# Kernel tuning notes

Hardware: AMD Instinct MI355X
Metric: run time of the kernel (lower is better)

The kernel has to match this reference:

```python
import jax, jax.numpy as jnp
import numpy as np

N_NODES = 100000
N_EDGES = 1600000
D_IN = 128
D_OUT = 128


def setup_inputs() -> dict:
    key = jax.random.key(0)
    k1, k2, k3, k4, k5 = jax.random.split(key, 5)
    x = jax.random.normal(k1, (N_NODES, D_IN), dtype=jnp.float32)
    edge_index = jax.random.randint(k2, (2, N_EDGES), 0, N_NODES, dtype=jnp.int32)
    edge_weight = jax.random.uniform(k3, (N_EDGES,), dtype=jnp.float32)
    # xavier-uniform linear weight [out, in]
    limit = float(np.sqrt(6.0 / (D_IN + D_OUT)))
    W = jax.random.uniform(k4, (D_OUT, D_IN), dtype=jnp.float32, minval=-limit, maxval=limit)
    bias = jnp.zeros((D_OUT,), dtype=jnp.float32)
    prelu_a = jax.random.uniform(k5, (1,), dtype=jnp.float32)
    return {"x": x, "edge_index": edge_index, "edge_weight": edge_weight,
            "W": W, "bias": bias, "prelu_a": prelu_a}


def _prelu(x, a):
    return jnp.where(x >= 0, x, a * x)


def reference(x, edge_index, edge_weight, W, bias, prelu_a):
    # seq_fts = fc(x): [N, D_OUT]
    h = x @ W.T
    # sparse adjacency matmul: out[dst] += w_e * h[src]
    src, dst = edge_index[0], edge_index[1]
    msgs = h[src] * edge_weight[:, None]          # [E, D_OUT]
    agg = jax.ops.segment_sum(msgs, dst, num_segments=N_NODES)
    out = agg + bias                              # bias add
    out = _prelu(out, prelu_a)                    # GCN's PReLU
    return jax.nn.relu(out)                       # GCNGeneration.activation
```

## Files before the change

kernel.cpp:

```cpp
#include <hip/hip_runtime.h>

#define N_NODES 100000
#define N_EDGES 1600000
#define D 128

#define NCB   512
#define BR    196
#define CHUNK 2048
#define SLOTS 8
#define CAP   4352

#define XQ   (N_NODES * D / 4)
#define XQB  (XQ / 256)
#define WQ   (D * D / 4)
#define WQB  (WQ / 256)
#define HB   256

typedef __bf16 bf16x8 __attribute__((ext_vector_type(8)));
typedef float  f32x4  __attribute__((ext_vector_type(4)));
typedef unsigned short u16x8 __attribute__((ext_vector_type(8)));

static __device__ __forceinline__ unsigned short f2bf(float f) {
    union { float f; unsigned u; } v; v.f = f;
    unsigned r = v.u + 0x7FFFu + ((v.u >> 16) & 1u);
    return (unsigned short)(r >> 16);
}

static __device__ __forceinline__ void accum_row(
    float4& acc0, float4& acc1, const float4 u, const float wt)
{
    const unsigned qx = __float_as_uint(u.x);
    const unsigned qy = __float_as_uint(u.y);
    const unsigned qz = __float_as_uint(u.z);
    const unsigned qw = __float_as_uint(u.w);
    acc0.x += wt * __uint_as_float(qx << 16);
    acc0.y += wt * __uint_as_float(qx & 0xFFFF0000u);
    acc0.z += wt * __uint_as_float(qy << 16);
    acc0.w += wt * __uint_as_float(qy & 0xFFFF0000u);
    acc1.x += wt * __uint_as_float(qz << 16);
    acc1.y += wt * __uint_as_float(qz & 0xFFFF0000u);
    acc1.z += wt * __uint_as_float(qw << 16);
    acc1.w += wt * __uint_as_float(qw & 0xFFFF0000u);
}

__global__ __launch_bounds__(256) void k_prep(
    const float4* __restrict__ x4, ushort4* __restrict__ xh4,
    const float4* __restrict__ w4, ushort4* __restrict__ wh4,
    const int* __restrict__ ei, int* __restrict__ ghist)
{
    __shared__ int h[NCB];
    const int b = blockIdx.x;
    const int t = threadIdx.x;
    if (b < HB) {
        h[t] = 0; h[t + 256] = 0;
        __syncthreads();
        for (int e = b * 256 + t; e < N_EDGES; e += HB * 256)
            atomicAdd(&h[ei[N_EDGES + e] / BR], 1);
        __syncthreads();
        atomicAdd(&ghist[t], h[t]);
        atomicAdd(&ghist[t + 256], h[t + 256]);
    } else if (b < HB + XQB) {
        const int i = (b - HB) * 256 + t;
        const float4 v = x4[i];
        xh4[i] = make_ushort4(f2bf(v.x), f2bf(v.y), f2bf(v.z), f2bf(v.w));
    } else {
        const int i = (b - HB - XQB) * 256 + t;
        const float4 v = w4[i];
        wh4[i] = make_ushort4(f2bf(v.x), f2bf(v.y), f2bf(v.z), f2bf(v.w));
    }
}

__global__ __launch_bounds__(512) void k_cscan(
    const int* __restrict__ ghist, int* __restrict__ cOff, int* __restrict__ gcur)
{
    __shared__ int sh[NCB];
    const int t = threadIdx.x;
    const int v = ghist[t];
    sh[t] = v;
    __syncthreads();
    for (int d = 1; d < NCB; d <<= 1) {
        int u = (t >= d) ? sh[t - d] : 0;
        __syncthreads();
        sh[t] += u;
        __syncthreads();
    }
    const int excl = sh[t] - v;
    cOff[t] = excl;
    gcur[t] = excl;
    if (t == NCB - 1) cOff[NCB] = sh[NCB - 1];
}

__global__ __launch_bounds__(256) void k_part(
    const int* __restrict__ ei, const float* __restrict__ ew,
    int* __restrict__ gcur, int2* __restrict__ part)
{
    __shared__ int2 bins[NCB * SLOTS];
    __shared__ int bcnt[NCB];
    __shared__ int bbase[NCB];
    const int t = threadIdx.x;
    const int e0 = blockIdx.x * CHUNK;

    bcnt[t] = 0; bcnt[t + 256] = 0;
    __syncthreads();

    #pragma unroll 8
    for (int k = 0; k < CHUNK / 256; ++k) {
        const int e = e0 + k * 256 + t;
        if (e < N_EDGES) {
            const int dst = ei[N_EDGES + e];
            const int src = ei[e];
            const int b = dst / BR;
            const int ld = dst - b * BR;
            const int2 p = make_int2(src | (ld << 17), __float_as_int(ew[e]));
            const int r = atomicAdd(&bcnt[b], 1);
            if (r < SLOTS) bins[b * SLOTS + r] = p;
            else {
                int pos = atomicAdd(&gcur[b], 1);
                part[pos] = p;
            }
        }
    }
    __syncthreads();

    {
        int c0 = min(bcnt[t], SLOTS);
        int c1 = min(bcnt[t + 256], SLOTS);
        bbase[t]       = c0 ? atomicAdd(&gcur[t], c0) : 0;
        bbase[t + 256] = c1 ? atomicAdd(&gcur[t + 256], c1) : 0;
        bcnt[t] = c0; bcnt[t + 256] = c1;
    }
    __syncthreads();

    for (int s = t; s < NCB * SLOTS; s += 256) {
        const int b = s >> 3;
        const int r = s & 7;
        if (r < bcnt[b]) part[bbase[b] + r] = bins[s];
    }
}

__global__ __launch_bounds__(256) void k_csr(
    const int* __restrict__ cOff, int2* __restrict__ part, int* __restrict__ off)
{
    __shared__ int2 buf[CAP];
    __shared__ int nh[256];
    __shared__ int orig[256];
    __shared__ int cur[256];

    const int b = blockIdx.x;
    const int t = threadIdx.x;
    const int lo = b * BR;
    const int base = cOff[b];
    int cnt = cOff[b + 1] - base;
    if (cnt > CAP) cnt = CAP;

    nh[t] = 0;
    __syncthreads();

    for (int i = t; i < cnt; i += 256) {
        const int2 p = part[base + i];
        buf[i] = p;
        atomicAdd(&nh[((unsigned)p.x) >> 17], 1);
    }
    __syncthreads();
    orig[t] = nh[t];
    __syncthreads();
    for (int d = 1; d < 256; d <<= 1) {
        int u = (t >= d) ? nh[t - d] : 0;
        __syncthreads();
        nh[t] += u;
        __syncthreads();
    }
    const int excl = nh[t] - orig[t];
    cur[t] = excl;
    if (t < BR && lo + t < N_NODES) off[lo + t] = base + excl;
    if (b == NCB - 1 && t == 0) off[N_NODES] = cOff[NCB];
    __syncthreads();

    for (int i = t; i < cnt; i += 256) {
        const int2 p = buf[i];
        const int ld = ((unsigned)p.x) >> 17;
        const int r = atomicAdd(&cur[ld], 1);
        part[base + r] = make_int2(p.x & 0x1FFFF, p.y);
    }
}

__global__ __launch_bounds__(256) void k_gx(
    const float4* __restrict__ xh4,
    const int* __restrict__ off,
    const int2* __restrict__ pair,
    const unsigned short* __restrict__ wh,
    const float* __restrict__ bias, const float* __restrict__ pa,
    float* __restrict__ out)
{
    __shared__ unsigned short tb[16][136];

    const int tid = threadIdx.x;
    const int g   = tid >> 4;
    const int sl  = tid & 15;
    const int m0  = blockIdx.x << 4;
    const float aP = pa[0];

    {
        const int n = m0 + g;
        const int beg = off[n], end = off[n + 1];
        float4 acc0 = make_float4(0.f, 0.f, 0.f, 0.f);
        float4 acc1 = make_float4(0.f, 0.f, 0.f, 0.f);

        int e = beg;
        for (; e + 3 < end; e += 4) {
            const int2 p0 = pair[e + 0], p1 = pair[e + 1];
            const int2 p2 = pair[e + 2], p3 = pair[e + 3];
            const float4 u0 = xh4[p0.x * 16 + sl];
            const float4 u1 = xh4[p1.x * 16 + sl];
            const float4 u2 = xh4[p2.x * 16 + sl];
            const float4 u3 = xh4[p3.x * 16 + sl];
            accum_row(acc0, acc1, u0, __int_as_float(p0.y));
            accum_row(acc0, acc1, u1, __int_as_float(p1.y));
            accum_row(acc0, acc1, u2, __int_as_float(p2.y));
            accum_row(acc0, acc1, u3, __int_as_float(p3.y));
        }
        for (; e < end; ++e) {
            const int2 p = pair[e];
            const float4 u = xh4[p.x * 16 + sl];
            accum_row(acc0, acc1, u, __int_as_float(p.y));
        }

        u16x8 s;
        s[0] = f2bf(acc0.x); s[1] = f2bf(acc0.y);
        s[2] = f2bf(acc0.z); s[3] = f2bf(acc0.w);
        s[4] = f2bf(acc1.x); s[5] = f2bf(acc1.y);
        s[6] = f2bf(acc1.z); s[7] = f2bf(acc1.w);
        *(u16x8*)&tb[g][sl * 8] = s;
    }
    __syncthreads();

    const int lane = tid & 63;
    const int wv = tid >> 6;
    const int mm = lane & 15;
    const int quad = lane >> 4;

    bf16x8 af[4];
    #pragma unroll
    for (int c = 0; c < 4; ++c)
        af[c] = *(const bf16x8*)&tb[mm][c * 32 + quad * 8];

    #pragma unroll
    for (int t = 0; t < 2; ++t) {
        const int n = ((wv * 2 + t) << 4) + mm;
        f32x4 acc = {0.f, 0.f, 0.f, 0.f};
        #pragma unroll
        for (int c = 0; c < 4; ++c) {
            const bf16x8 bf = *(const bf16x8*)(wh + n * D + c * 32 + quad * 8);
            acc = __builtin_amdgcn_mfma_f32_16x16x32_bf16(af[c], bf, acc, 0, 0, 0);
        }
        const float bv = bias[n];
        #pragma unroll
        for (int r = 0; r < 4; ++r) {
            float v = acc[r] + bv;
            v = (v >= 0.f) ? v : aP * v;
            v = fmaxf(v, 0.f);
            out[(size_t)(m0 + (quad << 2) + r) * D + n] = v;
        }
    }
}

__global__ __launch_bounds__(256) void gcn_scatter(
    const float* __restrict__ x, const int* __restrict__ ei,
    const float* __restrict__ ew, float* __restrict__ agg)
{
    const int lane = threadIdx.x & 63;
    const int wave = (blockIdx.x * blockDim.x + threadIdx.x) >> 6;
    const int nwaves = (gridDim.x * blockDim.x) >> 6;
    for (int e = wave; e < N_EDGES; e += nwaves) {
        const int src = ei[e];
        const int dst = ei[N_EDGES + e];
        const float w = ew[e];
        const float2 v = ((const float2*)(x + (size_t)src * D))[lane];
        float* op = agg + (size_t)dst * D + lane * 2;
        unsafeAtomicAdd(op,     w * v.x);
        unsafeAtomicAdd(op + 1, w * v.y);
    }
}

#define MT 32
__global__ __launch_bounds__(256, 2) void gcn_transform(
    const float* __restrict__ A, const float* __restrict__ W,
    const float* __restrict__ bias, const float* __restrict__ pa,
    float* __restrict__ out)
{
    __shared__ float Wt[D][D];
    __shared__ float xs[MT][D];
    const int tid = threadIdx.x;
    const int row0 = blockIdx.x * MT;

    for (int j = tid; j < D * (D / 4); j += 256) {
        const int n = j & 127;
        const int kg = j >> 7;
        const float4 v = ((const float4*)W)[n * (D / 4) + kg];
        const int k4 = kg << 2;
        Wt[k4 + 0][n] = v.x; Wt[k4 + 1][n] = v.y;
        Wt[k4 + 2][n] = v.z; Wt[k4 + 3][n] = v.w;
    }
    for (int i = tid; i < MT * (D / 4); i += 256) {
        const int r = i >> 5;
        const int c4 = i & 31;
        ((float4*)xs[r])[c4] = ((const float4*)(A + (size_t)(row0 + r) * D))[c4];
    }
    __syncthreads();

    const int tn = tid & 31;
    const int tm = tid >> 5;
    float acc[4][4] = {};
    #pragma unroll
    for (int k = 0; k < D; k += 4) {
        const float4 wv0 = *(const float4*)&Wt[k + 0][tn * 4];
        const float4 wv1 = *(const float4*)&Wt[k + 1][tn * 4];
        const float4 wv2 = *(const float4*)&Wt[k + 2][tn * 4];
        const float4 wv3 = *(const float4*)&Wt[k + 3][tn * 4];
        #pragma unroll
        for (int i = 0; i < 4; ++i) {
            const float4 xv = *(const float4*)&xs[tm * 4 + i][k];
            acc[i][0] += xv.x * wv0.x + xv.y * wv1.x + xv.z * wv2.x + xv.w * wv3.x;
            acc[i][1] += xv.x * wv0.y + xv.y * wv1.y + xv.z * wv2.y + xv.w * wv3.y;
            acc[i][2] += xv.x * wv0.z + xv.y * wv1.z + xv.z * wv2.z + xv.w * wv3.z;
            acc[i][3] += xv.x * wv0.w + xv.y * wv1.w + xv.z * wv2.w + xv.w * wv3.w;
        }
    }
    const float a = pa[0];
    const float4 bv = ((const float4*)bias)[tn];
    #pragma unroll
    for (int i = 0; i < 4; ++i) {
        const int gr = row0 + tm * 4 + i;
        float t0 = acc[i][0] + bv.x, t1 = acc[i][1] + bv.y;
        float t2 = acc[i][2] + bv.z, t3 = acc[i][3] + bv.w;
        float4 r;
        r.x = fmaxf(t0 >= 0.f ? t0 : a * t0, 0.f);
        r.y = fmaxf(t1 >= 0.f ? t1 : a * t1, 0.f);
        r.z = fmaxf(t2 >= 0.f ? t2 : a * t2, 0.f);
        r.w = fmaxf(t3 >= 0.f ? t3 : a * t3, 0.f);
        ((float4*)(out + (size_t)gr * D))[tn] = r;
    }
}

extern "C" void kernel_launch(void* const* d_in, const int* in_sizes, int n_in,
                              void* d_out, int out_size, void* d_ws, size_t ws_size,
                              hipStream_t stream) {
    const float* x    = (const float*)d_in[0];
    const int*   ei   = (const int*)d_in[1];
    const float* ew   = (const float*)d_in[2];
    const float* W    = (const float*)d_in[3];
    const float* bias = (const float*)d_in[4];
    const float* pa   = (const float*)d_in[5];
    float* out = (float*)d_out;

    const size_t o_ghist = 0;
    const size_t o_cOff  = o_ghist + NCB;
    const size_t o_gcur  = o_cOff + NCB + 1;
    const size_t o_off   = o_gcur + NCB;
    const size_t o_part  = o_off + N_NODES + 1;
    const size_t o_wh    = (o_part + 2 * (size_t)N_EDGES + 3) & ~(size_t)3;
    const size_t o_xh    = o_wh + (size_t)D * D / 2;
    const size_t endA    = o_xh + (size_t)N_NODES * D / 2;
    const size_t needA   = endA * 4;

    int* wsb = (int*)d_ws;
    int* ghist = wsb + o_ghist;
    int* cOff  = wsb + o_cOff;
    int* gcur  = wsb + o_gcur;
    int* off   = wsb + o_off;
    int2* part = (int2*)(wsb + o_part);
    unsigned short* wh = (unsigned short*)(wsb + o_wh);
    unsigned short* xh = (unsigned short*)(wsb + o_xh);

    if (ws_size >= needA) {
        (void)hipMemsetAsync(ghist, 0, NCB * sizeof(int), stream);
        k_prep <<<HB + XQB + WQB, 256, 0, stream>>>(
            (const float4*)x, (ushort4*)xh, (const float4*)W, (ushort4*)wh, ei, ghist);
        k_cscan<<<1, NCB, 0, stream>>>(ghist, cOff, gcur);
        k_part <<<(N_EDGES + CHUNK - 1) / CHUNK, 256, 0, stream>>>(ei, ew, gcur, part);
        k_csr  <<<NCB, 256, 0, stream>>>(cOff, part, off);
        k_gx   <<<N_NODES / 16, 256, 0, stream>>>(
            (const float4*)xh, off, part, wh, bias, pa, out);
    } else {
        (void)hipMemsetAsync(out, 0, (size_t)N_NODES * D * sizeof(float), stream);
        gcn_scatter<<<12800, 256, 0, stream>>>(x, ei, ew, out);
        gcn_transform<<<N_NODES / MT, 256, 0, stream>>>(out, W, bias, pa, out);
    }
}
```

Measured before the change: 267.5 us.

## Partition edges into fixed-capacity buckets to drop histogram and scan passes

Edges are binned by destination block straight into fixed-capacity per-bucket regions (CAPR slots each), so the separate destination histogram pass and the single-block prefix scan are no longer needed. Partitioning now runs in the same launch as the bf16 conversion of x and W. The CSR offsets become (begin,end) int2 pairs. This removes two kernel launches and one full read of the destination indices, but needs a larger workspace and silently drops edges if any bucket exceeds its capacity.

```diff
diff --git a/kernel.cpp b/kernel.cpp
--- a/kernel.cpp
+++ b/kernel.cpp
@@ -8,7 +8,10 @@
 #define BR    196
 #define CHUNK 2048
 #define SLOTS 8
+#define CAPR  4096
 #define CAP   4352
+#define LASTB ((N_NODES - 1) / BR)
+#define PBK   ((N_EDGES + CHUNK - 1) / CHUNK)
 
 #define XQ   (N_NODES * D / 4)
 #define XQB  (XQ / 256)
@@ -43,6 +46,114 @@
     acc1.w += wt * __uint_as_float(qw & 0xFFFF0000u);
 }
 
+
+__global__ __launch_bounds__(256) void k_pc(
+    const float4* __restrict__ x4, ushort4* __restrict__ xh4,
+    const float4* __restrict__ w4, ushort4* __restrict__ wh4,
+    const int* __restrict__ ei, const float* __restrict__ ew,
+    int* __restrict__ gcur, int2* __restrict__ part)
+{
+    __shared__ int2 bins[NCB * SLOTS];
+    __shared__ int bcnt[NCB];
+    __shared__ int bbase[NCB];
+    const int b = blockIdx.x;
+    const int t = threadIdx.x;
+
+    if (b < PBK) {
+        bcnt[t] = 0; bcnt[t + 256] = 0;
+        __syncthreads();
+        const int e0 = b * CHUNK;
+        #pragma unroll 8
+        for (int k = 0; k < CHUNK / 256; ++k) {
+            const int e = e0 + k * 256 + t;
+            if (e < N_EDGES) {
+                const int dst = ei[N_EDGES + e];
+                const int src = ei[e];
+                const int bk = dst / BR;
+                const int ld = dst - bk * BR;
+                const int2 p = make_int2(src | (ld << 17), __float_as_int(ew[e]));
+                const int r = atomicAdd(&bcnt[bk], 1);
+                if (r < SLOTS) bins[bk * SLOTS + r] = p;
+                else {
+                    const int pos = atomicAdd(&gcur[bk], 1);
+                    if (pos < CAPR) part[bk * CAPR + pos] = p;
+                }
+            }
+        }
+        __syncthreads();
+        {
+            const int c0 = min(bcnt[t], SLOTS);
+            const int c1 = min(bcnt[t + 256], SLOTS);
+            bbase[t]       = c0 ? atomicAdd(&gcur[t], c0) : 0;
+            bbase[t + 256] = c1 ? atomicAdd(&gcur[t + 256], c1) : 0;
+            bcnt[t] = c0; bcnt[t + 256] = c1;
+        }
+        __syncthreads();
+        for (int s = t; s < NCB * SLOTS; s += 256) {
+            const int bk = s >> 3;
+            const int r = s & 7;
+            if (r < bcnt[bk]) {
+                const int pos = bbase[bk] + r;
+                if (pos < CAPR) part[bk * CAPR + pos] = bins[s];
+            }
+        }
+    } else if (b < PBK + XQB) {
+        const int i = (b - PBK) * 256 + t;
+        const float4 v = x4[i];
+        xh4[i] = make_ushort4(f2bf(v.x), f2bf(v.y), f2bf(v.z), f2bf(v.w));
+    } else {
+        const int i = (b - PBK - XQB) * 256 + t;
+        const float4 v = w4[i];
+        wh4[i] = make_ushort4(f2bf(v.x), f2bf(v.y), f2bf(v.z), f2bf(v.w));
+    }
+}
+
+__global__ __launch_bounds__(256) void k_csrp(
+    const int* __restrict__ gcur, int2* __restrict__ part, int2* __restrict__ off2)
+{
+    __shared__ int2 buf[CAPR];
+    __shared__ int nh[256];
+    __shared__ int orig[256];
+    __shared__ int cur[256];
+
+    const int b = blockIdx.x;
+    const int t = threadIdx.x;
+    const int lo = b * BR;
+    const int base = b * CAPR;
+    int cnt = gcur[b];
+    if (cnt > CAPR) cnt = CAPR;
+
+    nh[t] = 0;
+    __syncthreads();
+
+    for (int i = t; i < cnt; i += 256) {
+        const int2 p = part[base + i];
+        buf[i] = p;
+        atomicAdd(&nh[((unsigned)p.x) >> 17], 1);
+    }
+    __syncthreads();
+    orig[t] = nh[t];
+    __syncthreads();
+    for (int d = 1; d < 256; d <<= 1) {
+        const int u = (t >= d) ? nh[t - d] : 0;
+        __syncthreads();
+        nh[t] += u;
+        __syncthreads();
+    }
+    const int excl = nh[t] - orig[t];
+    cur[t] = excl;
+    if (t < BR && lo + t < N_NODES)
+        off2[lo + t] = make_int2(base + excl, base + excl + orig[t]);
+    __syncthreads();
+
+    for (int i = t; i < cnt; i += 256) {
+        const int2 p = buf[i];
+        const int ld = ((unsigned)p.x) >> 17;
+        const int r = atomicAdd(&cur[ld], 1);
+        part[base + r] = make_int2(p.x & 0x1FFFF, p.y);
+    }
+}
+
 __global__ __launch_bounds__(256) void k_prep(
     const float4* __restrict__ x4, ushort4* __restrict__ xh4,
     const float4* __restrict__ w4, ushort4* __restrict__ wh4,
@@ -90,7 +201,7 @@
     if (t == NCB - 1) cOff[NCB] = sh[NCB - 1];
 }
 
-__global__ __launch_bounds__(256) void k_part(
+__global__ __launch_bounds__(256) void k_partc(
     const int* __restrict__ ei, const float* __restrict__ ew,
     int* __restrict__ gcur, int2* __restrict__ part)
 {
@@ -114,10 +225,7 @@
             const int2 p = make_int2(src | (ld << 17), __float_as_int(ew[e]));
             const int r = atomicAdd(&bcnt[b], 1);
             if (r < SLOTS) bins[b * SLOTS + r] = p;
-            else {
-                int pos = atomicAdd(&gcur[b], 1);
-                part[pos] = p;
-            }
+            else part[atomicAdd(&gcur[b], 1)] = p;
         }
     }
     __syncthreads();
@@ -138,8 +246,8 @@
     }
 }
 
-__global__ __launch_bounds__(256) void k_csr(
-    const int* __restrict__ cOff, int2* __restrict__ part, int* __restrict__ off)
+__global__ __launch_bounds__(256) void k_csrc(
+    const int* __restrict__ cOff, int2* __restrict__ part, int2* __restrict__ off2)
 {
     __shared__ int2 buf[CAP];
     __shared__ int nh[256];
@@ -172,8 +280,8 @@
     }
     const int excl = nh[t] - orig[t];
     cur[t] = excl;
-    if (t < BR && lo + t < N_NODES) off[lo + t] = base + excl;
-    if (b == NCB - 1 && t == 0) off[N_NODES] = cOff[NCB];
+    if (t < BR && lo + t < N_NODES)
+        off2[lo + t] = make_int2(base + excl, base + excl + orig[t]);
     __syncthreads();
 
     for (int i = t; i < cnt; i += 256) {
@@ -186,7 +294,7 @@
 
 __global__ __launch_bounds__(256) void k_gx(
     const float4* __restrict__ xh4,
-    const int* __restrict__ off,
+    const int2* __restrict__ off2,
     const int2* __restrict__ pair,
     const unsigned short* __restrict__ wh,
     const float* __restrict__ bias, const float* __restrict__ pa,
@@ -201,12 +309,12 @@
     const float aP = pa[0];
 
     {
-        const int n = m0 + g;
-        const int beg = off[n], end = off[n + 1];
+        const int2 oo = off2[m0 + g];
+        const int end = oo.y;
         float4 acc0 = make_float4(0.f, 0.f, 0.f, 0.f);
         float4 acc1 = make_float4(0.f, 0.f, 0.f, 0.f);
 
-        int e = beg;
+        int e = oo.x;
         for (; e + 3 < end; e += 4) {
             const int2 p0 = pair[e + 0], p1 = pair[e + 1];
             const int2 p2 = pair[e + 2], p3 = pair[e + 3];
@@ -352,35 +460,55 @@
     const float* bias = (const float*)d_in[4];
     const float* pa   = (const float*)d_in[5];
     float* out = (float*)d_out;
+    int* wsb = (int*)d_ws;
+
+    const size_t p_gcur = 0;
+    const size_t p_off2 = 512;
+    const size_t p_part = p_off2 + 2 * (size_t)N_NODES;
+    const size_t p_wh   = p_part + 2 * (size_t)NCB * CAPR;
+    const size_t p_xh   = p_wh + (size_t)D * D / 2;
+    const size_t needP  = (p_xh + (size_t)N_NODES * D / 2) * 4;
 
     const size_t o_ghist = 0;
-    const size_t o_cOff  = o_ghist + NCB;
-    const size_t o_gcur  = o_cOff + NCB + 1;
-    const size_t o_off   = o_gcur + NCB;
-    const size_t o_part  = o_off + N_NODES + 1;
+    const size_t o_cOff  = 512;
+    const size_t o_gcur  = 1025;
+    const size_t o_off2  = 1538;
+    const size_t o_part  = o_off2 + 2 * (size_t)N_NODES;
     const size_t o_wh    = (o_part + 2 * (size_t)N_EDGES + 3) & ~(size_t)3;
     const size_t o_xh    = o_wh + (size_t)D * D / 2;
-    const size_t endA    = o_xh + (size_t)N_NODES * D / 2;
-    const size_t needA   = endA * 4;
-
-    int* wsb = (int*)d_ws;
-    int* ghist = wsb + o_ghist;
-    int* cOff  = wsb + o_cOff;
-    int* gcur  = wsb + o_gcur;
-    int* off   = wsb + o_off;
-    int2* part = (int2*)(wsb + o_part);
-    unsigned short* wh = (unsigned short*)(wsb + o_wh);
-    unsigned short* xh = (unsigned short*)(wsb + o_xh);
-
-    if (ws_size >= needA) {
+    const size_t needA   = (o_xh + (size_t)N_NODES * D / 2) * 4;
+
+    if (ws_size >= needP) {
+        int* gcur  = wsb + p_gcur;
+        int2* off2 = (int2*)(wsb + p_off2);
+        int2* part = (int2*)(wsb + p_part);
+        unsigned short* wh = (unsigned short*)(wsb + p_wh);
+        unsigned short* xh = (unsigned short*)(wsb + p_xh);
+
+        (void)hipMemsetAsync(gcur, 0, NCB * sizeof(int), stream);
+        k_pc  <<<PBK + XQB + WQB, 256, 0, stream>>>(
+            (const float4*)x, (ushort4*)xh, (const float4*)W, (ushort4*)wh,
+            ei, ew, gcur, part);
+        k_csrp<<<NCB, 256, 0, stream>>>(gcur, part, off2);
+        k_gx  <<<N_NODES / 16, 256, 0, stream>>>(
+            (const float4*)xh, off2, part, wh, bias, pa, out);
+    } else if (ws_size >= needA) {
+        int* ghist = wsb + o_ghist;
+        int* cOff  = wsb + o_cOff;
+        int* gcur  = wsb + o_gcur;
+        int2* off2 = (int2*)(wsb + o_off2);
+        int2* part = (int2*)(wsb + o_part);
+        unsigned short* wh = (unsigned short*)(wsb + o_wh);
+        unsigned short* xh = (unsigned short*)(wsb + o_xh);
+
         (void)hipMemsetAsync(ghist, 0, NCB * sizeof(int), stream);
         k_prep <<<HB + XQB + WQB, 256, 0, stream>>>(
             (const float4*)x, (ushort4*)xh, (const float4*)W, (ushort4*)wh, ei, ghist);
         k_cscan<<<1, NCB, 0, stream>>>(ghist, cOff, gcur);
-        k_part <<<(N_EDGES + CHUNK - 1) / CHUNK, 256, 0, stream>>>(ei, ew, gcur, part);
-        k_csr  <<<NCB, 256, 0, stream>>>(cOff, part, off);
+        k_partc<<<PBK, 256, 0, stream>>>(ei, ew, gcur, part);
+        k_csrc <<<NCB, 256, 0, stream>>>(cOff, part, off2);
         k_gx   <<<N_NODES / 16, 256, 0, stream>>>(
-            (const float4*)xh, off, part, wh, bias, pa, out);
+            (const float4*)xh, off2, part, wh, bias, pa, out);
     } else {
         (void)hipMemsetAsync(out, 0, (size_t)N_NODES * D * sizeof(float), stream);
         gcn_scatter<<<12800, 256, 0, stream>>>(x, ei, ew, out);
```

Measured after the change: 232.1 us. 1.15x faster.
